# Kernel optimization log

Measured on AMD Instinct MI355X. Metric: run time of the kernel, lower is better.

## Reference

```python
import jax, jax.numpy as jnp
import numpy as np

B, N = 2, 512
D_NODE, D_EDGE, D_HID, H = 128, 64, 128, 8
DH = D_HID // H  # per-head dim = 16
SCALE = 1.0 / (D_HID ** 0.5)  # note: scale uses full d_hid as in source


def setup_inputs() -> dict:
    key = jax.random.key(0)
    k1, k2, k3, k4 = jax.random.split(key, 4)
    node_features = jax.random.normal(k1, (B, N, D_NODE), dtype=jnp.float32)
    edge_features = jax.random.normal(k2, (B, N, N, D_EDGE), dtype=jnp.float32)
    mask = jnp.ones((B, N, N), dtype=bool)
    # Linear weights (stored as (in, out); math identical to torch x @ W.T)
    W_node = jax.random.normal(k3, (D_NODE, 3 * D_HID), dtype=jnp.float32) / np.sqrt(D_NODE)
    W_edge = jax.random.normal(k4, (D_EDGE, 3 * D_HID), dtype=jnp.float32) / np.sqrt(D_EDGE)
    return {"node_features": node_features, "edge_features": edge_features,
            "mask": mask, "W_node": W_node, "W_edge": W_edge}


def _split_heads_node(x):
    # (b, n, h*c) -> (b, h, n, c)
    b, n, hc = x.shape
    return x.reshape(b, n, H, hc // H).transpose(0, 2, 1, 3)


def _split_heads_edge(x):
    # (b, n, m, h*c) -> (b, h, n, m, c)
    b, n, m, hc = x.shape
    return x.reshape(b, n, m, H, hc // H).transpose(0, 3, 1, 2, 4)


def reference(node_features, edge_features, mask, W_node, W_edge):
    # node qkv: (b, n, 3*d_hid) -> (b, h, n, 3*dh) -> chunk
    qkv_n = _split_heads_node(node_features @ W_node)
    q_node, k_node, v_node = jnp.split(qkv_n, 3, axis=-1)  # each (b,h,n,dh)
    # edge qkv: (b, n, n, 3*d_hid) -> (b, h, n, n, 3*dh) -> chunk
    qkv_e = _split_heads_edge(edge_features @ W_edge)
    q_edge, k_edge, v_edge = jnp.split(qkv_e, 3, axis=-1)  # each (b,h,n,n,dh)

    q = q_node[:, :, :, None, :] + q_edge   # (b,h,i,j,dh)
    k = k_node[:, :, None, :, :] + k_edge   # (b,h,i,j,dh)
    v = v_node[:, :, None, :, :] + v_edge   # (b,h,i,j,dh)

    dots = SCALE * jnp.einsum('bhijd,bhijd->bhij', q, k)
    attn = jax.nn.softmax(dots, axis=-1)
    out = jnp.einsum('bhij,bhijd->bhid', attn, v)  # (b,h,n,dh)
    # (b,h,n,dh) -> (b,n,h*dh)
    b, h, n, dh = out.shape
    return out.transpose(0, 2, 1, 3).reshape(b, n, h * dh)
```

## Files before the change

### kernel.cpp

```cpp
#include <hip/hip_runtime.h>
#include <hip/hip_bf16.h>

#define NN 512
#define OC 384
#define S2F 0.12751694f

typedef __attribute__((ext_vector_type(8))) short short8;
typedef __attribute__((ext_vector_type(4))) float f32x4;

#define LD4(p) (*reinterpret_cast<const f32x4*>(p))

__device__ __forceinline__ unsigned short f2bf(float x) {
    unsigned u = __builtin_bit_cast(unsigned, x);
    u = (u + 0x7fffu + ((u >> 16) & 1u)) >> 16;
    return (unsigned short)u;
}

__device__ __forceinline__ short8 cvt8(f32x4 a, f32x4 b) {
    union { short8 s8; __hip_bfloat162 h[4]; } r;
    r.h[0] = __float22bfloat162_rn(make_float2(a[0], a[1]));
    r.h[1] = __float22bfloat162_rn(make_float2(a[2], a[3]));
    r.h[2] = __float22bfloat162_rn(make_float2(b[0], b[1]));
    r.h[3] = __float22bfloat162_rn(make_float2(b[2], b[3]));
    return r.s8;
}

__device__ __forceinline__ void gl_lds16(const float* g, float* l) {
    __builtin_amdgcn_global_load_lds(
        (const __attribute__((address_space(1))) void*)g,
        (__attribute__((address_space(3))) void*)l,
        16, 0, 0);
}

__global__ __launch_bounds__(256) void prep0_kernel(
    const float* __restrict__ Wn, const float* __restrict__ We,
    const float* __restrict__ node,
    unsigned short* __restrict__ WtN, unsigned short* __restrict__ WtE,
    unsigned short* __restrict__ nodeBf)
{
    int idx = blockIdx.x * 256 + threadIdx.x;
    if (idx < 24576) {
        int o = idx >> 6, k = idx & 63;
        WtE[idx] = f2bf(We[k * OC + o]);
    } else if (idx < 24576 + 49152) {
        int id = idx - 24576;
        int o = id >> 7, k = id & 127;
        WtN[id] = f2bf(Wn[k * OC + o]);
    } else {
        int id = idx - 73728;
        nodeBf[id] = f2bf(node[id]);
    }
}

__global__ __launch_bounds__(256) void prep1_kernel(
    const unsigned short* __restrict__ nodeBf,
    const unsigned short* __restrict__ WtN,
    float* __restrict__ qnF,
    float* __restrict__ nodeKV)
{
    const int t = threadIdx.x;
    const int w = t >> 6;
    const int lane = t & 63;
    const int lj = lane & 15;
    const int quad = lane >> 4;
    const int nbase = blockIdx.x * 32;

    short8 bfr[2][4];
#pragma unroll
    for (int nt = 0; nt < 2; ++nt)
#pragma unroll
        for (int ks = 0; ks < 4; ++ks)
            bfr[nt][ks] = *reinterpret_cast<const short8*>(
                nodeBf + (size_t)(nbase + nt * 16 + lj) * 128 + ks * 32 + quad * 8);

#pragma unroll
    for (int m = 0; m < 6; ++m) {
        int ot = (6 * w + m) * 16;
        short8 afr[4];
#pragma unroll
        for (int ks = 0; ks < 4; ++ks)
            afr[ks] = *reinterpret_cast<const short8*>(
                WtN + (size_t)(ot + lj) * 128 + ks * 32 + quad * 8);
#pragma unroll
        for (int nt = 0; nt < 2; ++nt) {
            f32x4 acc = {0.f, 0.f, 0.f, 0.f};
#pragma unroll
            for (int ks = 0; ks < 4; ++ks)
                acc = __builtin_amdgcn_mfma_f32_16x16x32_bf16(afr[ks], bfr[nt][ks], acc, 0, 0, 0);
            int n = nbase + nt * 16 + lj;
            int bb = n >> 9, ii = n & 511;
#pragma unroll
            for (int r = 0; r < 4; ++r) {
                int o = ot + quad * 4 + r;
                int h = o / 48, rem = o - h * 48;
                if (rem < 16) {
                    qnF[((size_t)(bb * 8 + h) * NN + ii) * 16 + rem] = acc[r];
                } else {
                    int d = (rem - 16) & 15;
                    int kv = (rem >= 32) ? 1 : 0;
                    size_t slot = ((((size_t)(bb * 8 + h) * 4 + (d >> 2)) * 2 + kv) * NN + ii) * 4 + (d & 3);
                    nodeKV[slot] = acc[r];
                }
            }
        }
    }
}

__global__ __launch_bounds__(512, 2) void rt_attn_main(
    const float* __restrict__ edge,
    const float* __restrict__ qnF,
    const float* __restrict__ nodeKV,
    const unsigned short* __restrict__ WtE,
    float* __restrict__ oaP,
    float* __restrict__ lP)
{
    __shared__ __align__(16) float sE[4 * 64 * 64];
    const int blk = blockIdx.x;
    const int jt = blk & 7;
    const int ic = (blk >> 3) & 127;
    const int b  = blk >> 10;
    const int i0 = ic * 4;
    const int t = threadIdx.x;
    const int h = t >> 6;
    const int lane = t & 63;
    const int lj = lane & 15;
    const int quad = lane >> 4;

    {
        const int rL = lane >> 4;
        const int cP = lane & 15;
#pragma unroll
        for (int m = 0; m < 8; ++m) {
            const int chunk = h * 8 + m;
            const int T  = chunk >> 4;
            const int r  = (chunk & 15) * 4 + rL;
            const int cl = (cP - r) & 15;
            const float* src = edge
                + ((size_t)(b * NN + i0 + T) * NN + jt * 64 + r) * 64 + cl * 4;
            gl_lds16(src, &sE[chunk * 256]);
        }
    }

    const float* kvB = nodeKV + ((size_t)(b * 8 + h) * 4 + quad) * (2 * NN * 4) + (size_t)lj * 4;
    f32x4 ka[4], va[4];
#pragma unroll
    for (int jn = 0; jn < 4; ++jn) {
        const float* kvp = kvB + (size_t)(jt * 64 + jn * 16) * 4;
        ka[jn] = LD4(kvp);
        va[jn] = LD4(kvp + NN * 4);
    }

    const float* qB = qnF + ((size_t)(b * 8 + h) * NN + i0) * 16 + quad * 4;
    f32x4 qnr[4];
#pragma unroll
    for (int ii = 0; ii < 4; ++ii) qnr[ii] = LD4(qB + ii * 16);

    short8 afr[3][2];
#pragma unroll
    for (int T = 0; T < 3; ++T)
#pragma unroll
        for (int sec = 0; sec < 2; ++sec)
            afr[T][sec] = *reinterpret_cast<const short8*>(
                WtE + (size_t)(h * 48 + T * 16 + lj) * 64 + sec * 32 + quad * 8);

    const int po0 = (((2 * quad)     + lj) & 15) * 4;
    const int po1 = (((2 * quad + 1) + lj) & 15) * 4;
    const int po2 = (((2 * quad + 8) + lj) & 15) * 4;
    const int po3 = (((2 * quad + 9) + lj) & 15) * 4;

    asm volatile("s_waitcnt vmcnt(0)" ::: "memory");
    __syncthreads();

#pragma unroll
    for (int ii = 0; ii < 4; ++ii) {
        const f32x4 qn = qnr[ii];
        float dp[4];
        f32x4 fvv[4];
#pragma unroll
        for (int jn = 0; jn < 4; ++jn) {
            const float* rb = &sE[ii * 4096 + (jn * 16 + lj) * 64];
            short8 b0 = cvt8(LD4(rb + po0), LD4(rb + po1));
            short8 b1 = cvt8(LD4(rb + po2), LD4(rb + po3));
            f32x4 fq = qn;
            fq = __builtin_amdgcn_mfma_f32_16x16x32_bf16(afr[0][0], b0, fq, 0, 0, 0);
            fq = __builtin_amdgcn_mfma_f32_16x16x32_bf16(afr[0][1], b1, fq, 0, 0, 0);
            f32x4 fk = ka[jn];
            fk = __builtin_amdgcn_mfma_f32_16x16x32_bf16(afr[1][0], b0, fk, 0, 0, 0);
            fk = __builtin_amdgcn_mfma_f32_16x16x32_bf16(afr[1][1], b1, fk, 0, 0, 0);
            f32x4 fv = va[jn];
            fv = __builtin_amdgcn_mfma_f32_16x16x32_bf16(afr[2][0], b0, fv, 0, 0, 0);
            fv = __builtin_amdgcn_mfma_f32_16x16x32_bf16(afr[2][1], b1, fv, 0, 0, 0);
            fvv[jn] = fv;
            float d0 = fq[0] * fk[0];
            d0 = fmaf(fq[1], fk[1], d0);
            d0 = fmaf(fq[2], fk[2], d0);
            d0 = fmaf(fq[3], fk[3], d0);
            dp[jn] = d0;
        }
        float t16[4], t32[4], wg[4];
        float l = 0.f;
#pragma unroll
        for (int jn = 0; jn < 4; ++jn) t16[jn] = __shfl_xor(dp[jn], 16);
#pragma unroll
        for (int jn = 0; jn < 4; ++jn) dp[jn] += t16[jn];
#pragma unroll
        for (int jn = 0; jn < 4; ++jn) t32[jn] = __shfl_xor(dp[jn], 32);
#pragma unroll
        for (int jn = 0; jn < 4; ++jn) {
            wg[jn] = exp2f((dp[jn] + t32[jn]) * S2F);
            l += wg[jn];
        }
        float oa[4] = {0.f, 0.f, 0.f, 0.f};
#pragma unroll
        for (int jn = 0; jn < 4; ++jn)
#pragma unroll
            for (int r = 0; r < 4; ++r)
                oa[r] = fmaf(wg[jn], fvv[jn][r], oa[r]);
#pragma unroll
        for (int off = 1; off <= 8; off <<= 1) {
            l += __shfl_xor(l, off);
#pragma unroll
            for (int r = 0; r < 4; ++r) oa[r] += __shfl_xor(oa[r], off);
        }
        if (lj == 0) {
            size_t pbase = ((size_t)(b * 8 + h) * 8 + jt) * NN + (i0 + ii);
            f32x4 o4;
#pragma unroll
            for (int r = 0; r < 4; ++r) o4[r] = oa[r];
            *reinterpret_cast<f32x4*>(oaP + pbase * 16 + quad * 4) = o4;
            if (quad == 0) lP[pbase] = l;
        }
    }
}

__global__ __launch_bounds__(256) void combine_kernel(
    const float* __restrict__ oaP,
    const float* __restrict__ lP,
    float* __restrict__ out)
{
    int tid = blockIdx.x * 256 + threadIdx.x;
    int d = tid & 15;
    int i = (tid >> 4) & 511;
    int h = (tid >> 13) & 7;
    int b = tid >> 16;
    float num = 0.f, den = 0.f;
#pragma unroll
    for (int jt = 0; jt < 8; ++jt) {
        size_t pb = ((size_t)(b * 8 + h) * 8 + jt) * NN + i;
        num += oaP[pb * 16 + d];
        den += lP[pb];
    }
    out[((size_t)b * NN + i) * 128 + h * 16 + d] = num / den;
}

extern "C" void kernel_launch(void* const* d_in, const int* in_sizes, int n_in,
                              void* d_out, int out_size, void* d_ws, size_t ws_size,
                              hipStream_t stream) {
    const float* node = (const float*)d_in[0];
    const float* edge = (const float*)d_in[1];
    const float* Wn = (const float*)d_in[3];
    const float* We = (const float*)d_in[4];
    float* out = (float*)d_out;

    char* ws = (char*)d_ws;
    float* qnF = (float*)ws;
    float* nodeKV = (float*)(ws + 524288);
    unsigned short* WtE = (unsigned short*)(ws + 1572864);
    unsigned short* WtN = (unsigned short*)(ws + 1622016);
    unsigned short* nodeBf = (unsigned short*)(ws + 1720320);
    float* oaP = (float*)(ws + 2097152);
    float* lP  = (float*)(ws + 6291456);

    prep0_kernel<<<800, 256, 0, stream>>>(Wn, We, node, WtN, WtE, nodeBf);
    prep1_kernel<<<32, 256, 0, stream>>>(nodeBf, WtN, qnF, nodeKV);
    rt_attn_main<<<2 * 128 * 8, 512, 0, stream>>>(edge, qnF, nodeKV, WtE, oaP, lP);
    combine_kernel<<<512, 256, 0, stream>>>(oaP, lP, out);
}
```

Measured before the change: 221.5 us.

## Double-buffer edge tiles in LDS with fewer, longer-running attention blocks

The main attention kernel now launches 512 blocks instead of 2048. Each block processes 16 query rows in 8 stages of 2 rows. Edge tiles are double-buffered in LDS through global_load_lds, so the next stage's loads overlap compute on the current one, and the q-node rows are staged in LDS once per block. This hides global-memory latency and amortises the K/V and weight fragment loads across more rows. In exchange it uses more LDS per block, adds per-stage barriers, and relies on hand-counted vmcnt waits that must stay exact.

```diff
diff --git a/kernel.cpp b/kernel.cpp
--- a/kernel.cpp
+++ b/kernel.cpp
@@ -9,6 +9,7 @@
 typedef __attribute__((ext_vector_type(4))) float f32x4;
 
 #define LD4(p) (*reinterpret_cast<const f32x4*>(p))
+#define SCHED_FENCE() __builtin_amdgcn_sched_barrier(0)
 
 __device__ __forceinline__ unsigned short f2bf(float x) {
     unsigned u = __builtin_bit_cast(unsigned, x);
@@ -114,47 +115,48 @@
     float* __restrict__ oaP,
     float* __restrict__ lP)
 {
-    __shared__ __align__(16) float sE[4 * 64 * 64];
+    __shared__ __align__(16) float sE[2][8192];
+    __shared__ __align__(16) float sQ[2048];
     const int blk = blockIdx.x;
-    const int jt = blk & 7;
-    const int ic = (blk >> 3) & 127;
-    const int b  = blk >> 10;
-    const int i0 = ic * 4;
+    const int jt  = blk >> 6;
+    const int g   = blk & 63;
+    const int b   = g >> 5;
+    const int gg  = g & 31;
     const int t = threadIdx.x;
     const int h = t >> 6;
     const int lane = t & 63;
     const int lj = lane & 15;
     const int quad = lane >> 4;
-
-    {
-        const int rL = lane >> 4;
-        const int cP = lane & 15;
-#pragma unroll
-        for (int m = 0; m < 8; ++m) {
-            const int chunk = h * 8 + m;
+    const int rL = lane >> 4;
+    const int cP = lane & 15;
+
+    auto stage = [&](int sIdx, int hf) {
+#pragma unroll
+        for (int m = 0; m < 4; ++m) {
+            const int chunk = h * 4 + m;
             const int T  = chunk >> 4;
             const int r  = (chunk & 15) * 4 + rL;
             const int cl = (cP - r) & 15;
+            const int i  = gg * 16 + sIdx * 2 + T;
             const float* src = edge
-                + ((size_t)(b * NN + i0 + T) * NN + jt * 64 + r) * 64 + cl * 4;
-            gl_lds16(src, &sE[chunk * 256]);
+                + ((size_t)(b * NN + i) * NN + jt * 64 + r) * 64 + cl * 4;
+            gl_lds16(src, &sE[hf][chunk * 256]);
         }
-    }
-
-    const float* kvB = nodeKV + ((size_t)(b * 8 + h) * 4 + quad) * (2 * NN * 4) + (size_t)lj * 4;
+    };
+
+    stage(0, 0);
+    gl_lds16(qnF + ((size_t)(b * 8 + h) * NN + gg * 16) * 16 + lane * 4,
+             &sQ[h * 256]);
+    SCHED_FENCE();
+    const float* kvB = nodeKV + ((size_t)(b * 8 + h) * 4 + quad) * (2 * NN * 4)
+                     + (size_t)(jt * 64) * 4 + (size_t)lj * 4;
     f32x4 ka[4], va[4];
 #pragma unroll
     for (int jn = 0; jn < 4; ++jn) {
-        const float* kvp = kvB + (size_t)(jt * 64 + jn * 16) * 4;
+        const float* kvp = kvB + (size_t)(jn * 16) * 4;
         ka[jn] = LD4(kvp);
         va[jn] = LD4(kvp + NN * 4);
     }
-
-    const float* qB = qnF + ((size_t)(b * 8 + h) * NN + i0) * 16 + quad * 4;
-    f32x4 qnr[4];
-#pragma unroll
-    for (int ii = 0; ii < 4; ++ii) qnr[ii] = LD4(qB + ii * 16);
-
     short8 afr[3][2];
 #pragma unroll
     for (int T = 0; T < 3; ++T)
@@ -162,73 +164,93 @@
         for (int sec = 0; sec < 2; ++sec)
             afr[T][sec] = *reinterpret_cast<const short8*>(
                 WtE + (size_t)(h * 48 + T * 16 + lj) * 64 + sec * 32 + quad * 8);
+    SCHED_FENCE();
+    stage(1, 1);
+    SCHED_FENCE();
+    asm volatile("s_waitcnt vmcnt(4)" ::: "memory");
+    SCHED_FENCE();
+    __builtin_amdgcn_s_barrier();
+    SCHED_FENCE();
 
     const int po0 = (((2 * quad)     + lj) & 15) * 4;
     const int po1 = (((2 * quad + 1) + lj) & 15) * 4;
     const int po2 = (((2 * quad + 8) + lj) & 15) * 4;
     const int po3 = (((2 * quad + 9) + lj) & 15) * 4;
 
-    asm volatile("s_waitcnt vmcnt(0)" ::: "memory");
-    __syncthreads();
-
-#pragma unroll
-    for (int ii = 0; ii < 4; ++ii) {
-        const f32x4 qn = qnr[ii];
-        float dp[4];
-        f32x4 fvv[4];
-#pragma unroll
-        for (int jn = 0; jn < 4; ++jn) {
-            const float* rb = &sE[ii * 4096 + (jn * 16 + lj) * 64];
-            short8 b0 = cvt8(LD4(rb + po0), LD4(rb + po1));
-            short8 b1 = cvt8(LD4(rb + po2), LD4(rb + po3));
-            f32x4 fq = qn;
-            fq = __builtin_amdgcn_mfma_f32_16x16x32_bf16(afr[0][0], b0, fq, 0, 0, 0);
-            fq = __builtin_amdgcn_mfma_f32_16x16x32_bf16(afr[0][1], b1, fq, 0, 0, 0);
-            f32x4 fk = ka[jn];
-            fk = __builtin_amdgcn_mfma_f32_16x16x32_bf16(afr[1][0], b0, fk, 0, 0, 0);
-            fk = __builtin_amdgcn_mfma_f32_16x16x32_bf16(afr[1][1], b1, fk, 0, 0, 0);
-            f32x4 fv = va[jn];
-            fv = __builtin_amdgcn_mfma_f32_16x16x32_bf16(afr[2][0], b0, fv, 0, 0, 0);
-            fv = __builtin_amdgcn_mfma_f32_16x16x32_bf16(afr[2][1], b1, fv, 0, 0, 0);
-            fvv[jn] = fv;
-            float d0 = fq[0] * fk[0];
-            d0 = fmaf(fq[1], fk[1], d0);
-            d0 = fmaf(fq[2], fk[2], d0);
-            d0 = fmaf(fq[3], fk[3], d0);
-            dp[jn] = d0;
+    for (int s = 0; s < 8; ++s) {
+        const int hf = s & 1;
+#pragma unroll
+        for (int rr = 0; rr < 2; ++rr) {
+            const f32x4 qn = LD4(&sQ[h * 256 + (s * 2 + rr) * 16 + quad * 4]);
+            float dp[4];
+            f32x4 fvv[4];
+#pragma unroll
+            for (int jn = 0; jn < 4; ++jn) {
+                const float* rb = &sE[hf][rr * 4096 + (jn * 16 + lj) * 64];
+                short8 b0 = cvt8(LD4(rb + po0), LD4(rb + po1));
+                short8 b1 = cvt8(LD4(rb + po2), LD4(rb + po3));
+                f32x4 fq = qn;
+                fq = __builtin_amdgcn_mfma_f32_16x16x32_bf16(afr[0][0], b0, fq, 0, 0, 0);
+                fq = __builtin_amdgcn_mfma_f32_16x16x32_bf16(afr[0][1], b1, fq, 0, 0, 0);
+                f32x4 fk = ka[jn];
+                fk = __builtin_amdgcn_mfma_f32_16x16x32_bf16(afr[1][0], b0, fk, 0, 0, 0);
+                fk = __builtin_amdgcn_mfma_f32_16x16x32_bf16(afr[1][1], b1, fk, 0, 0, 0);
+                f32x4 fv = va[jn];
+                fv = __builtin_amdgcn_mfma_f32_16x16x32_bf16(afr[2][0], b0, fv, 0, 0, 0);
+                fv = __builtin_amdgcn_mfma_f32_16x16x32_bf16(afr[2][1], b1, fv, 0, 0, 0);
+                fvv[jn] = fv;
+                float d0 = fq[0] * fk[0];
+                d0 = fmaf(fq[1], fk[1], d0);
+                d0 = fmaf(fq[2], fk[2], d0);
+                d0 = fmaf(fq[3], fk[3], d0);
+                dp[jn] = d0;
+            }
+            float t16[4], t32[4], wg[4];
+            float l = 0.f;
+#pragma unroll
+            for (int jn = 0; jn < 4; ++jn) t16[jn] = __shfl_xor(dp[jn], 16);
+#pragma unroll
+            for (int jn = 0; jn < 4; ++jn) dp[jn] += t16[jn];
+#pragma unroll
+            for (int jn = 0; jn < 4; ++jn) t32[jn] = __shfl_xor(dp[jn], 32);
+#pragma unroll
+            for (int jn = 0; jn < 4; ++jn) {
+                wg[jn] = exp2f((dp[jn] + t32[jn]) * S2F);
+                l += wg[jn];
+            }
+            float oa[4] = {0.f, 0.f, 0.f, 0.f};
+#pragma unroll
+            for (int jn = 0; jn < 4; ++jn)
+#pragma unroll
+                for (int r = 0; r < 4; ++r)
+                    oa[r] = fmaf(wg[jn], fvv[jn][r], oa[r]);
+#pragma unroll
+            for (int off = 1; off <= 8; off <<= 1) {
+                l += __shfl_xor(l, off);
+#pragma unroll
+                for (int r = 0; r < 4; ++r) oa[r] += __shfl_xor(oa[r], off);
+            }
+            if (lj == 0) {
+                const int i = gg * 16 + s * 2 + rr;
+                size_t pbase = ((size_t)(b * 8 + h) * 8 + jt) * NN + i;
+                f32x4 o4;
+#pragma unroll
+                for (int r = 0; r < 4; ++r) o4[r] = oa[r];
+                *reinterpret_cast<f32x4*>(oaP + pbase * 16 + quad * 4) = o4;
+                if (quad == 0) lP[pbase] = l;
+            }
         }
-        float t16[4], t32[4], wg[4];
-        float l = 0.f;
-#pragma unroll
-        for (int jn = 0; jn < 4; ++jn) t16[jn] = __shfl_xor(dp[jn], 16);
-#pragma unroll
-        for (int jn = 0; jn < 4; ++jn) dp[jn] += t16[jn];
-#pragma unroll
-        for (int jn = 0; jn < 4; ++jn) t32[jn] = __shfl_xor(dp[jn], 32);
-#pragma unroll
-        for (int jn = 0; jn < 4; ++jn) {
-            wg[jn] = exp2f((dp[jn] + t32[jn]) * S2F);
-            l += wg[jn];
-        }
-        float oa[4] = {0.f, 0.f, 0.f, 0.f};
-#pragma unroll
-        for (int jn = 0; jn < 4; ++jn)
-#pragma unroll
-            for (int r = 0; r < 4; ++r)
-                oa[r] = fmaf(wg[jn], fvv[jn][r], oa[r]);
-#pragma unroll
-        for (int off = 1; off <= 8; off <<= 1) {
-            l += __shfl_xor(l, off);
-#pragma unroll
-            for (int r = 0; r < 4; ++r) oa[r] += __shfl_xor(oa[r], off);
-        }
-        if (lj == 0) {
-            size_t pbase = ((size_t)(b * 8 + h) * 8 + jt) * NN + (i0 + ii);
-            f32x4 o4;
-#pragma unroll
-            for (int r = 0; r < 4; ++r) o4[r] = oa[r];
-            *reinterpret_cast<f32x4*>(oaP + pbase * 16 + quad * 4) = o4;
-            if (quad == 0) lP[pbase] = l;
+        if (s < 7) {
+            asm volatile("s_waitcnt lgkmcnt(0)" ::: "memory");
+            SCHED_FENCE();
+            __builtin_amdgcn_s_barrier();
+            SCHED_FENCE();
+            if (s < 6) stage(s + 2, hf);
+            SCHED_FENCE();
+            asm volatile("s_waitcnt vmcnt(4)" ::: "memory");
+            SCHED_FENCE();
+            __builtin_amdgcn_s_barrier();
+            SCHED_FENCE();
         }
     }
 }
@@ -273,6 +295,6 @@
 
     prep0_kernel<<<800, 256, 0, stream>>>(Wn, We, node, WtN, WtE, nodeBf);
     prep1_kernel<<<32, 256, 0, stream>>>(nodeBf, WtN, qnF, nodeKV);
-    rt_attn_main<<<2 * 128 * 8, 512, 0, stream>>>(edge, qnF, nodeKV, WtE, oaP, lP);
+    rt_attn_main<<<512, 512, 0, stream>>>(edge, qnF, nodeKV, WtE, oaP, lP);
     combine_kernel<<<512, 256, 0, stream>>>(oaP, lP, out);
 }
```

New measurement: 225.1 us. No clear change (+1.6%).
